# Kernel tuning notes

Measured on AMD Instinct MI355X. Metric: run time of the kernel, lower is better.

The kernel has to match this reference:

```python
import jax, jax.numpy as jnp
import numpy as np

B, N, T, CIN = 16, 400, 12, 2
HID, H, D = 256, 8, 32
P, EMB, TOPK, K = 3, 10, 16, 3


def _conv1d(x, w, b, dil):
    # x: (BN, C, T), w: (O, I, K); causal (left) padding like F.pad((pad,0))
    pad = (K - 1) * dil
    y = jax.lax.conv_general_dilated(x, w, (1,), [(pad, 0)], rhs_dilation=(dil,),
                                     dimension_numbers=('NCH', 'OIH', 'NCH'))
    return y + b[None, :, None]


def _ln(x, g, b):
    m = x.mean(-1, keepdims=True)
    v = x.var(-1, keepdims=True)
    return (x - m) / jnp.sqrt(v + 1e-5) * g + b


def setup_inputs() -> dict:
    key = jax.random.key(0)
    kit = iter(jax.random.split(key, 64))

    def g(shape, s=0.05):
        return jax.random.normal(next(kit), shape, jnp.float32) * s

    # fixed graph: ring with 8 neighbors + self loop -> L = 9*N edges
    idx = np.arange(N)
    offs = np.array([-4, -3, -2, -1, 0, 1, 2, 3, 4])
    recv = np.repeat(idx, offs.size)
    send = (recv + np.tile(offs, N)) % N
    L = recv.size

    inp = {
        'x': g((B, N, T, CIN), 1.0),
        'edge_feat': g((B, L, 2), 1.0),
        'fixed_edge_index': jnp.asarray(np.stack([recv, send]).astype(np.int32)),
        # GTCN layer 0 (dilation 1): gate/filter/skip convs + LayerNorm
        'wg0': g((HID, CIN, K)), 'bg0': jnp.zeros((HID,), jnp.float32),
        'wf0': g((HID, CIN, K)), 'bf0': jnp.zeros((HID,), jnp.float32),
        'ws0': g((HID, CIN, K)), 'bs0': jnp.zeros((HID,), jnp.float32),
        'ln0g': jnp.ones((HID,), jnp.float32), 'ln0b': jnp.zeros((HID,), jnp.float32),
        # GTCN layer 1 (dilation 2)
        'wg1': g((HID, HID, K)), 'bg1': jnp.zeros((HID,), jnp.float32),
        'wf1': g((HID, HID, K)), 'bf1': jnp.zeros((HID,), jnp.float32),
        'ws1': g((HID, HID, K)), 'bs1': jnp.zeros((HID,), jnp.float32),
        'ln1g': jnp.ones((HID,), jnp.float32), 'ln1b': jnp.zeros((HID,), jnp.float32),
        'wsk': g((CIN, HID)), 'bsk': jnp.zeros((HID,), jnp.float32),
        # sparse GAT on fixed physical graph (with 2-dim edge features)
        'sWq': g((HID, HID)), 'sWk': g((HID, HID)), 'sWv': g((HID, HID)),
        'sWe': g((2, HID)),
        'saq': g((H, D)), 'sak': g((H, D)), 'sae': g((H, D)),
        # dense GAT on adaptive adjacency
        'dWq': g((HID, HID)), 'dWk': g((HID, HID)), 'dWv': g((HID, HID)),
        'daq': g((H, D)), 'dak': g((H, D)),
        'E1': g((N, EMB), 0.5), 'E2': g((N, EMB), 0.5),
        # gated fusion
        'fW1': g((HID, HID)), 'fb1': jnp.zeros((HID,), jnp.float32),
        'fW2': g((HID, HID)), 'fb2': jnp.zeros((HID,), jnp.float32),
        'fW3': g((HID, HID)), 'fb3': jnp.zeros((HID,), jnp.float32),
        # prediction head
        'Wo': g((HID, P)), 'bo': jnp.zeros((P,), jnp.float32),
    }
    return inp


def reference(x, edge_feat,
              wg0, bg0, wf0, bf0, ws0, bs0, ln0g, ln0b,
              wg1, bg1, wf1, bf1, ws1, bs1, ln1g, ln1b, wsk, bsk,
              sWq, sWk, sWv, sWe, saq, sak, sae,
              dWq, dWk, dWv, daq, dak, E1, E2,
              fW1, fb1, fW2, fb2, fW3, fb3, Wo, bo,
              fixed_edge_index):
    Bb, Nn, Tt, _ = x.shape
    # ---- GTCN (gated temporal conv stack with residual skip) ----
    res = x @ wsk + bsk                                   # (B,N,T,HID)
    xc = x.reshape(Bb * Nn, Tt, -1).transpose(0, 2, 1)    # (BN,C,T)
    for (wg, bg, wf, bf, ws, bs, lg, lb), dil in (
            ((wg0, bg0, wf0, bf0, ws0, bs0, ln0g, ln0b), 1),
            ((wg1, bg1, wf1, bf1, ws1, bs1, ln1g, ln1b), 2)):
        gate = jax.nn.sigmoid(_conv1d(xc, wg, bg, dil))
        y = gate * _conv1d(xc, wf, bf, dil) + (1 - gate) * _conv1d(xc, ws, bs, dil)
        y = jax.nn.relu(_ln(y.transpose(0, 2, 1), lg, lb))  # (BN,T,HID)
        xc = y.transpose(0, 2, 1)
    h = xc.transpose(0, 2, 1).reshape(Bb, Nn, Tt, HID) + res
    hl = h[:, :, -1, :]                                   # (B,N,HID) last step

    # ---- sparse GAT on fixed physical graph (edge features) ----
    recv, send = fixed_edge_index[0], fixed_edge_index[1]
    q = (hl @ sWq).reshape(Bb, Nn, H, D)
    k = (hl @ sWk).reshape(Bb, Nn, H, D)
    v = (hl @ sWv).reshape(Bb, Nn, H, D)
    e = (edge_feat @ sWe).reshape(Bb, -1, H, D)
    s = (q[:, recv] * saq).sum(-1) + (k[:, send] * sak).sum(-1) + (e * sae).sum(-1)
    s = jax.nn.leaky_relu(s, 0.2)                         # (B,L,H)
    mx = jnp.full((Bb, Nn, H), -jnp.inf, s.dtype).at[:, recv].max(s)
    ex = jnp.exp(s - mx[:, recv])
    den = jnp.zeros((Bb, Nn, H), s.dtype).at[:, recv].add(ex)
    alpha = ex / jnp.clip(den[:, recv], 1e-12, None)
    agg = jnp.zeros((Bb, Nn, H, D), v.dtype).at[:, recv].add(alpha[..., None] * v[:, send])
    h_fixed = jax.nn.elu(agg.reshape(Bb, Nn, HID))

    # ---- dense GAT on adaptive (learned, top-k sparsified) adjacency ----
    A = jax.nn.softmax(jax.nn.relu(E1 @ E2.T), axis=-1)   # (N,N)
    kth = jax.lax.top_k(A, TOPK)[0][:, -1:]
    adj_adp = jnp.where(A >= kth, A, 0.0)
    q = (hl @ dWq).reshape(Bb, Nn, H, D)
    k = (hl @ dWk).reshape(Bb, Nn, H, D)
    v = (hl @ dWv).reshape(Bb, Nn, H, D)
    sc = (q * daq).sum(-1)[:, :, None, :] + (k * dak).sum(-1)[:, None, :, :]  # (B,N,N,H)
    sc = jax.nn.leaky_relu(sc, 0.2)
    sc = sc + jnp.log(jnp.clip(adj_adp, 1e-12, None))[None, :, :, None]      # log-adj trick
    sc = jnp.where((adj_adp > 0)[None, :, :, None], sc, -1e9)
    al = jax.nn.softmax(sc, axis=2)
    h_adp = jax.nn.elu(jnp.einsum('bnjh,bjhd->bnhd', al, v).reshape(Bb, Nn, HID))

    # ---- gated fusion + prediction head ----
    gate = jax.nn.sigmoid((h_fixed + h_adp) @ fW1 + fb1)
    fused = jnp.tanh(gate * (h_fixed @ fW2 + fb2) + (1 - gate) * (h_adp @ fW3 + fb3))
    return fused @ Wo + bo                                # (B,N,P)
```

## Files before the change

### kernel.cpp

```cpp
#include <hip/hip_runtime.h>
#include <math.h>

#define LL 3600
#define NODES 6400

typedef __attribute__((ext_vector_type(8))) _Float16 half8;
typedef __attribute__((ext_vector_type(4))) float f32x4;
typedef __attribute__((ext_vector_type(4))) unsigned short ushort4v;

__device__ __forceinline__ unsigned short f2h(float f) {
    union { _Float16 h; unsigned short u; } cv;
    cv.h = (_Float16)f;
    return cv.u;
}
__device__ __forceinline__ float h2f(unsigned short u) {
    union { unsigned short u; _Float16 h; } cv;
    cv.u = u;
    return (float)cv.h;
}

#define GLOAD16(gp, lp) __builtin_amdgcn_global_load_lds( \
    (const __attribute__((address_space(1))) unsigned int*)(const void*)(gp), \
    (__attribute__((address_space(3))) unsigned int*)(void*)(lp), 16, 0, 0)

__global__ __launch_bounds__(256) void prep_kernel(
    const float* __restrict__ wg1, const float* __restrict__ wf1, const float* __restrict__ ws1,
    const float* __restrict__ sWv, const float* __restrict__ dWv,
    const float* __restrict__ sWq, const float* __restrict__ saq,
    const float* __restrict__ sWk, const float* __restrict__ sak,
    const float* __restrict__ dWq, const float* __restrict__ daq,
    const float* __restrict__ dWk, const float* __restrict__ dak,
    const float* __restrict__ fW1, const float* __restrict__ fW2, const float* __restrict__ fW3,
    const float* __restrict__ sWe, const float* __restrict__ sae,
    const float* __restrict__ E1, const float* __restrict__ E2,
    const float* __restrict__ x,
    const float* __restrict__ wg0, const float* __restrict__ bg0,
    const float* __restrict__ wf0, const float* __restrict__ bf0,
    const float* __restrict__ ws0, const float* __restrict__ bs0,
    const float* __restrict__ lg0, const float* __restrict__ lb0,
    const float* __restrict__ bo,
    unsigned short* __restrict__ W1h,
    unsigned short* __restrict__ W2h,
    unsigned short* __restrict__ W3h,
    float* __restrict__ AeS,
    int* __restrict__ cnt, int* __restrict__ idxs, float* __restrict__ logv,
    unsigned short* __restrict__ Xh,
    float* __restrict__ out) {
    int bid = blockIdx.x;
    int tid = threadIdx.x;

    if (bid < 2304) {
        int idx = bid * 256 + tid;
        int n = idx / 768, k = idx % 768;
        int which = n >> 8, o = n & 255;
        int tt = k >> 8, i = k & 255;
        const float* w = which == 0 ? wg1 : (which == 1 ? wf1 : ws1);
        W1h[idx] = f2h(w[(o * 256 + i) * 3 + tt]);
    } else if (bid < 2944) {
        int idx = (bid - 2304) * 256 + tid;
        int n = idx / 256, k = idx % 256;
        float v = 0.f;
        if (n < 256) v = sWv[k * 256 + n];
        else if (n < 512) v = dWv[k * 256 + (n - 256)];
        else if (n < 544) {
            int j = n - 512, g = j >> 3, h = j & 7;
            const float* Wm = g == 0 ? sWq : (g == 1 ? sWk : (g == 2 ? dWq : dWk));
            const float* am = g == 0 ? saq : (g == 1 ? sak : (g == 2 ? daq : dak));
            float s = 0.f;
            for (int d = 0; d < 32; d++) s += Wm[k * 256 + h * 32 + d] * am[h * 32 + d];
            v = s;
        }
        W2h[idx] = f2h(v);
    } else if (bid < 4480) {
        int idx = (bid - 2944) * 256 + tid;
        int n = idx / 512, k = idx % 512;
        float v = 0.f;
        if (k < 256) {
            if (n < 256) v = fW1[k * 256 + n];
            else if (n < 512) v = fW2[k * 256 + (n - 256)];
        } else {
            int c = k - 256;
            if (n < 256) v = fW1[c * 256 + n];
            else if (n >= 512) v = fW3[c * 256 + (n - 512)];
        }
        W3h[idx] = f2h(v);
    } else if (bid == 4480) {
        if (tid < 16) {
            int cc = tid / 8, h = tid % 8;
            float s = 0.f;
            for (int d = 0; d < 32; d++) s += sWe[cc * 256 + h * 32 + d] * sae[h * 32 + d];
            AeS[tid] = s;
        }
    } else if (bid < 4581) {
        int n = ((bid - 4481) * 256 + tid) >> 6;
        int lane = tid & 63;
        if (n >= 400) return;
        float e1[10];
        #pragma unroll
        for (int k = 0; k < 10; k++) e1[k] = E1[n * 10 + k];
        float p[7];
        #pragma unroll
        for (int i = 0; i < 7; i++) {
            int j = i * 64 + lane;
            if (j < 400) {
                float s = 0.f;
                #pragma unroll
                for (int k = 0; k < 10; k++) s += e1[k] * E2[j * 10 + k];
                p[i] = fmaxf(s, 0.f);
            } else p[i] = -1e30f;
        }
        float mx = -1e30f;
        #pragma unroll
        for (int i = 0; i < 7; i++) mx = fmaxf(mx, p[i]);
        #pragma unroll
        for (int o = 32; o > 0; o >>= 1) mx = fmaxf(mx, __shfl_xor(mx, o, 64));
        float sum = 0.f;
        #pragma unroll
        for (int i = 0; i < 7; i++) {
            int j = i * 64 + lane;
            if (j < 400) { p[i] = expf(p[i] - mx); sum += p[i]; }
        }
        #pragma unroll
        for (int o = 32; o > 0; o >>= 1) sum += __shfl_xor(sum, o, 64);
        float inv = 1.f / sum;
        float m[7];
        #pragma unroll
        for (int i = 0; i < 7; i++) {
            int j = i * 64 + lane;
            if (j < 400) { p[i] *= inv; m[i] = p[i]; }
            else m[i] = -1e30f;
        }
        for (int it = 0; it < 15; ++it) {
            float lm = m[0];
            #pragma unroll
            for (int i = 1; i < 7; i++) lm = fmaxf(lm, m[i]);
            float gm = lm;
            #pragma unroll
            for (int o = 32; o > 0; o >>= 1) gm = fmaxf(gm, __shfl_xor(gm, o, 64));
            unsigned long long msk = __ballot(lm == gm);
            int first = (int)(__ffsll((long long)msk)) - 1;
            if (lane == first) {
                #pragma unroll
                for (int i = 0; i < 7; i++) {
                    if (m[i] == gm) { m[i] = -1e30f; break; }
                }
            }
        }
        float kth = m[0];
        #pragma unroll
        for (int i = 1; i < 7; i++) kth = fmaxf(kth, m[i]);
        #pragma unroll
        for (int o = 32; o > 0; o >>= 1) kth = fmaxf(kth, __shfl_xor(kth, o, 64));
        int base = 0;
        #pragma unroll
        for (int i = 0; i < 7; i++) {
            int j = i * 64 + lane;
            bool pred = (j < 400) && (p[i] >= kth);
            unsigned long long msk = __ballot(pred);
            int pre = __popcll(msk & ((lane == 63) ? 0x7fffffffffffffffull : ((1ull << lane) - 1)));
            if (pred) {
                int pos = base + pre;
                if (pos < 64) {
                    idxs[n * 64 + pos] = j;
                    logv[n * 64 + pos] = logf(fmaxf(p[i], 1e-12f));
                }
            }
            base += __popcll(msk);
        }
        if (lane == 0) cnt[n] = base < 64 ? base : 64;
    } else if (bid < 6181) {
        int lane = tid & 63;
        int node = (bid - 4581) * 4 + (tid >> 6);
        float xs[14];
        #pragma unroll
        for (int t = 0; t < 7; t++) {
            xs[t * 2]     = x[(size_t)(node * 12 + 5 + t) * 2];
            xs[t * 2 + 1] = x[(size_t)(node * 12 + 5 + t) * 2 + 1];
        }
        float wg[4][6], wf[4][6], wsv[4][6], bgv[4], bfv[4], bsv[4], gln[4], bln[4];
        #pragma unroll
        for (int cc = 0; cc < 4; cc++) {
            int o = lane * 4 + cc;
            #pragma unroll
            for (int i = 0; i < 6; i++) {
                wg[cc][i] = wg0[o * 6 + i];
                wf[cc][i] = wf0[o * 6 + i];
                wsv[cc][i] = ws0[o * 6 + i];
            }
            bgv[cc] = bg0[o]; bfv[cc] = bf0[o]; bsv[cc] = bs0[o];
            gln[cc] = lg0[o]; bln[cc] = lb0[o];
        }
        #pragma unroll
        for (int tt = 0; tt < 3; tt++) {
            int tb = 2 * tt;
            float y[4];
            float s1 = 0.f, s2 = 0.f;
            #pragma unroll
            for (int cc = 0; cc < 4; cc++) {
                float g = bgv[cc], f = bfv[cc], s = bsv[cc];
                #pragma unroll
                for (int k = 0; k < 3; k++) {
                    #pragma unroll
                    for (int c = 0; c < 2; c++) {
                        float xv = xs[(tb + k) * 2 + c];
                        g += wg[cc][c * 3 + k] * xv;
                        f += wf[cc][c * 3 + k] * xv;
                        s += wsv[cc][c * 3 + k] * xv;
                    }
                }
                float gate = 1.f / (1.f + expf(-g));
                y[cc] = gate * f + (1.f - gate) * s;
                s1 += y[cc];
                s2 += y[cc] * y[cc];
            }
            #pragma unroll
            for (int o = 32; o > 0; o >>= 1) {
                s1 += __shfl_xor(s1, o, 64);
                s2 += __shfl_xor(s2, o, 64);
            }
            float mean = s1 * (1.f / 256.f);
            float var = s2 * (1.f / 256.f) - mean * mean;
            float rstd = rsqrtf(var + 1e-5f);
            unsigned short h4[4];
            #pragma unroll
            for (int cc = 0; cc < 4; cc++) {
                float v = (y[cc] - mean) * rstd * gln[cc] + bln[cc];
                h4[cc] = f2h(fmaxf(v, 0.f));
            }
            unsigned long long pack = (unsigned long long)h4[0] | ((unsigned long long)h4[1] << 16)
                                    | ((unsigned long long)h4[2] << 32) | ((unsigned long long)h4[3] << 48);
            *(unsigned long long*)&Xh[(size_t)node * 768 + tt * 256 + lane * 4] = pack;
        }
    } else {
        int idx = (bid - 6181) * 256 + tid;
        if (idx < NODES * 3) out[idx] = bo[idx % 3];
    }
}

template<int K, int LDC, int GX, int GY>
__global__ __launch_bounds__(256, 4) void gemm_f16_big(
    const unsigned short* __restrict__ A,
    const unsigned short* __restrict__ BT,
    unsigned short* __restrict__ C) {
    __shared__ __align__(16) unsigned short lA[3][128 * 32];
    __shared__ __align__(16) unsigned short lB[3][64 * 32];
    int tid = threadIdx.x;
    int lane = tid & 63;
    int w = tid >> 6;
    int wm = w >> 1, wn = w & 1;
    int r = lane & 15, g4 = lane >> 4;

    constexpr int NWG = GX * GY;
    constexpr int Q = NWG / 8, R = NWG % 8;
    int flat = blockIdx.y * GX + blockIdx.x;
    int xcd = flat & 7, idx = flat >> 3;
    int nf = (xcd < R ? xcd * (Q + 1) : R * (Q + 1) + (xcd - R) * Q) + idx;
    int col0 = (nf % GX) * 64;
    int row0 = (nf / GX) * 128;

    f32x4 acc[4][2] = {};

    int rS = tid >> 2;
    int slot = tid & 3;
    int tkA0 = (slot ^ (rS & 3)) * 8;
    int tkA1 = (slot ^ ((rS + 64) & 3)) * 8;
    int tkB = tkA0;

#define STAGE(sel, kk) do { \
    GLOAD16(A + (size_t)(row0 + rS) * K + (kk) + tkA0, &lA[sel][tid * 8]); \
    GLOAD16(A + (size_t)(row0 + 64 + rS) * K + (kk) + tkA1, &lA[sel][(tid + 256) * 8]); \
    GLOAD16(BT + (size_t)(col0 + rS) * K + (kk) + tkB, &lB[sel][tid * 8]); \
} while (0)

    int sw = (g4 ^ (r & 3)) << 3;

#define COMPUTE(cur) do { \
    half8 a_[4], b_[2]; \
    _Pragma("unroll") \
    for (int mi = 0; mi < 4; ++mi) \
        a_[mi] = *(const half8*)&lA[cur][(wm * 64 + mi * 16 + r) * 32 + sw]; \
    _Pragma("unroll") \
    for (int ni = 0; ni < 2; ++ni) \
        b_[ni] = *(const half8*)&lB[cur][(wn * 32 + ni * 16 + r) * 32 + sw]; \
    _Pragma("unroll") \
    for (int mi = 0; mi < 4; ++mi) \
        _Pragma("unroll") \
        for (int ni = 0; ni < 2; ++ni) \
            acc[mi][ni] = __builtin_amdgcn_mfma_f32_16x16x32_f16(a_[mi], b_[ni], acc[mi][ni], 0, 0, 0); \
} while (0)

    constexpr int NT = K >> 5;
    STAGE(0, 0);
    STAGE(1, 32);
    for (int t = 0; t < NT - 1; ++t) {
        asm volatile("s_waitcnt vmcnt(3)" ::: "memory");
        __builtin_amdgcn_s_barrier();
        if (t + 2 < NT) STAGE((t + 2) % 3, (t + 2) * 32);
        COMPUTE(t % 3);
    }
    asm volatile("s_waitcnt vmcnt(0)" ::: "memory");
    __builtin_amdgcn_s_barrier();
    COMPUTE((NT - 1) % 3);
#undef STAGE
#undef COMPUTE

    #pragma unroll
    for (int mi = 0; mi < 4; ++mi) {
        #pragma unroll
        for (int ni = 0; ni < 2; ++ni) {
            int rowb = row0 + wm * 64 + mi * 16 + g4 * 4;
            int colb = col0 + wn * 32 + ni * 16 + r;
            #pragma unroll
            for (int j = 0; j < 4; ++j)
                C[(size_t)(rowb + j) * LDC + colb] = f2h(acc[mi][ni][j]);
        }
    }
}

__global__ __launch_bounds__(256, 3) void gemm3_fused(
    const unsigned short* __restrict__ A,
    const unsigned short* __restrict__ BT,
    const float* __restrict__ fb1, const float* __restrict__ fb2, const float* __restrict__ fb3,
    const float* __restrict__ Wo,
    float* __restrict__ out) {
    __shared__ __align__(16) unsigned short lA[3][64 * 32];
    __shared__ __align__(16) unsigned short lB[3][3][64 * 32];
    int tid = threadIdx.x;
    int lane = tid & 63;
    int w = tid >> 6;
    int wm = w >> 1, wn = w & 1;
    int r = lane & 15, g4 = lane >> 4;

    constexpr int NWG = 400;
    constexpr int Q = NWG / 8;
    int flat = blockIdx.y * 4 + blockIdx.x;
    int xcd = flat & 7, idx = flat >> 3;
    int nf = xcd * Q + idx;
    int c0 = (nf % 4) * 64;
    int row0 = (nf / 4) * 64;

    f32x4 acc[3][2][2] = {};

    int rS = tid >> 2;
    int slot = tid & 3;
    int tk = (slot ^ (rS & 3)) * 8;

#define STAGE3(sel, kk) do { \
    GLOAD16(A + (size_t)(row0 + rS) * 512 + (kk) + tk, &lA[sel][tid * 8]); \
    GLOAD16(BT + (size_t)(c0 + rS) * 512 + (kk) + tk, &lB[sel][0][tid * 8]); \
    GLOAD16(BT + (size_t)(c0 + 256 + rS) * 512 + (kk) + tk, &lB[sel][1][tid * 8]); \
    GLOAD16(BT + (size_t)(c0 + 512 + rS) * 512 + (kk) + tk, &lB[sel][2][tid * 8]); \
} while (0)

    int sw = (g4 ^ (r & 3)) << 3;

#define COMPUTE3(cur) do { \
    half8 a_[2], b_[3][2]; \
    _Pragma("unroll") \
    for (int mi = 0; mi < 2; ++mi) \
        a_[mi] = *(const half8*)&lA[cur][(wm * 32 + mi * 16 + r) * 32 + sw]; \
    _Pragma("unroll") \
    for (int q = 0; q < 3; ++q) \
        _Pragma("unroll") \
        for (int ni = 0; ni < 2; ++ni) \
            b_[q][ni] = *(const half8*)&lB[cur][q][(wn * 32 + ni * 16 + r) * 32 + sw]; \
    _Pragma("unroll") \
    for (int q = 0; q < 3; ++q) \
        _Pragma("unroll") \
        for (int mi = 0; mi < 2; ++mi) \
            _Pragma("unroll") \
            for (int ni = 0; ni < 2; ++ni) \
                acc[q][mi][ni] = __builtin_amdgcn_mfma_f32_16x16x32_f16(a_[mi], b_[q][ni], acc[q][mi][ni], 0, 0, 0); \
} while (0)

    constexpr int NT = 16;
    STAGE3(0, 0);
    STAGE3(1, 32);
    for (int t = 0; t < NT - 1; ++t) {
        asm volatile("s_waitcnt vmcnt(4)" ::: "memory");
        __builtin_amdgcn_s_barrier();
        if (t + 2 < NT) STAGE3((t + 2) % 3, (t + 2) * 32);
        COMPUTE3(t % 3);
    }
    asm volatile("s_waitcnt vmcnt(0)" ::: "memory");
    __builtin_amdgcn_s_barrier();
    COMPUTE3((NT - 1) % 3);
#undef STAGE3
#undef COMPUTE3

    #pragma unroll
    for (int mi = 0; mi < 2; ++mi) {
        float v0[4] = {}, v1[4] = {}, v2[4] = {};
        #pragma unroll
        for (int ni = 0; ni < 2; ++ni) {
            int ch = c0 + wn * 32 + ni * 16 + r;
            float b1 = fb1[ch], b2 = fb2[ch], b3 = fb3[ch];
            float w0 = Wo[ch * 3 + 0], w1 = Wo[ch * 3 + 1], w2 = Wo[ch * 3 + 2];
            #pragma unroll
            for (int j = 0; j < 4; ++j) {
                float g = 1.f / (1.f + expf(-(acc[0][mi][ni][j] + b1)));
                float a2 = acc[1][mi][ni][j] + b2;
                float a3 = acc[2][mi][ni][j] + b3;
                float fused = tanhf(g * a2 + (1.f - g) * a3);
                v0[j] += fused * w0;
                v1[j] += fused * w1;
                v2[j] += fused * w2;
            }
        }
        #pragma unroll
        for (int off = 1; off < 16; off <<= 1) {
            #pragma unroll
            for (int j = 0; j < 4; ++j) {
                v0[j] += __shfl_xor(v0[j], off, 64);
                v1[j] += __shfl_xor(v1[j], off, 64);
                v2[j] += __shfl_xor(v2[j], off, 64);
            }
        }
        if (r == 0) {
            int rowb = row0 + wm * 32 + mi * 16 + g4 * 4;
            #pragma unroll
            for (int j = 0; j < 4; ++j) {
                atomicAdd(&out[(size_t)(rowb + j) * 3 + 0], v0[j]);
                atomicAdd(&out[(size_t)(rowb + j) * 3 + 1], v1[j]);
                atomicAdd(&out[(size_t)(rowb + j) * 3 + 2], v2[j]);
            }
        }
    }
}

__global__ __launch_bounds__(256) void epi1_kernel(
    const unsigned short* __restrict__ Y1, const float* __restrict__ x,
    const float* __restrict__ bg1, const float* __restrict__ bf1, const float* __restrict__ bs1,
    const float* __restrict__ lg, const float* __restrict__ lb,
    const float* __restrict__ wsk, const float* __restrict__ bsk,
    unsigned short* __restrict__ HLh) {
    int lane = threadIdx.x & 63;
    int node = blockIdx.x * 4 + (threadIdx.x >> 6);
    size_t base = (size_t)node * 768;
    ushort4v yg = *(const ushort4v*)&Y1[base + lane * 4];
    ushort4v yf = *(const ushort4v*)&Y1[base + 256 + lane * 4];
    ushort4v ys = *(const ushort4v*)&Y1[base + 512 + lane * 4];
    float y[4];
    float s1 = 0.f, s2 = 0.f;
    #pragma unroll
    for (int cc = 0; cc < 4; cc++) {
        int o = lane * 4 + cc;
        float g = h2f(yg[cc]) + bg1[o];
        float f = h2f(yf[cc]) + bf1[o];
        float s = h2f(ys[cc]) + bs1[o];
        float gate = 1.f / (1.f + expf(-g));
        y[cc] = gate * f + (1.f - gate) * s;
        s1 += y[cc];
        s2 += y[cc] * y[cc];
    }
    #pragma unroll
    for (int off = 32; off > 0; off >>= 1) {
        s1 += __shfl_xor(s1, off, 64);
        s2 += __shfl_xor(s2, off, 64);
    }
    float mean = s1 * (1.f / 256.f);
    float var = s2 * (1.f / 256.f) - mean * mean;
    float rstd = rsqrtf(var + 1e-5f);
    float x0 = x[(size_t)(node * 12 + 11) * 2];
    float x1 = x[(size_t)(node * 12 + 11) * 2 + 1];
    unsigned short h4[4];
    #pragma unroll
    for (int cc = 0; cc < 4; cc++) {
        int o = lane * 4 + cc;
        float v = (y[cc] - mean) * rstd * lg[o] + lb[o];
        v = fmaxf(v, 0.f);
        float res = x0 * wsk[o] + x1 * wsk[256 + o] + bsk[o];
        h4[cc] = f2h(v + res);
    }
    unsigned long long pack = (unsigned long long)h4[0] | ((unsigned long long)h4[1] << 16)
                            | ((unsigned long long)h4[2] << 32) | ((unsigned long long)h4[3] << 48);
    *(unsigned long long*)&HLh[(size_t)node * 256 + lane * 4] = pack;
}

__global__ __launch_bounds__(256) void gat_kernel(
    const unsigned short* __restrict__ Y2, const float* __restrict__ ef,
    const int* __restrict__ fei, const float* __restrict__ AeS,
    const int* __restrict__ cnt, const int* __restrict__ idxs, const float* __restrict__ logv,
    unsigned short* __restrict__ Uh) {
    int node = (blockIdx.x & 7) * 800 + (blockIdx.x >> 3);
    int b = node / 400, n = node % 400;
    int tid = threadIdx.x;
    __shared__ int snd[9];
    __shared__ float alf[9][8];
    __shared__ float invdf[8];
    __shared__ int jidx[64];
    __shared__ float sca[64][8];
    __shared__ float alb[64][8];
    __shared__ float invda[8];
    __shared__ float svf[9][8];
    int c = cnt[n];

    if (tid < 64) {
        int lane = tid;
        if (lane < 9) snd[lane] = fei[LL + n * 9 + lane];
        for (int e = lane; e < 72; e += 64) {
            int j = e >> 3, h = e & 7;
            int l = n * 9 + j;
            float e0 = ef[((size_t)b * LL + l) * 2];
            float e1 = ef[((size_t)b * LL + l) * 2 + 1];
            float ae = e0 * AeS[h] + e1 * AeS[8 + h];
            float aq = h2f(Y2[(size_t)node * 640 + 512 + h]);
            float ak = h2f(Y2[((size_t)(b * 400 + snd[j])) * 640 + 520 + h]);
            float s = aq + ak + ae;
            svf[j][h] = s > 0.f ? s : 0.2f * s;
        }
        if (lane < 8) {
            int h = lane;
            float mx = -1e30f;
            #pragma unroll
            for (int j = 0; j < 9; j++) mx = fmaxf(mx, svf[j][h]);
            float den = 0.f;
            #pragma unroll
            for (int j = 0; j < 9; j++) { float e = expf(svf[j][h] - mx); alf[j][h] = e; den += e; }
            invdf[h] = 1.f / fmaxf(den, 1e-12f);
        }
    } else if (tid < 128) {
        int lane = tid - 64;
        if (lane < c) jidx[lane] = idxs[n * 64 + lane];
        float jl = (lane < c) ? logv[n * 64 + lane] : 0.f;
        for (int e = lane; e < c * 8; e += 64) {
            int j = e >> 3, h = e & 7;
            float aq = h2f(Y2[(size_t)node * 640 + 528 + h]);
            float ak = h2f(Y2[((size_t)(b * 400 + jidx[j])) * 640 + 536 + h]);
            float s = aq + ak;
            s = s > 0.f ? s : 0.2f * s;
            sca[j][h] = s + __shfl(jl, j, 64);
        }
        int h = lane >> 3, grp = lane & 7;
        float mx = -1e30f;
        for (int j = grp; j < c; j += 8) mx = fmaxf(mx, sca[j][h]);
        #pragma unroll
        for (int o = 1; o < 8; o <<= 1) mx = fmaxf(mx, __shfl_xor(mx, o, 64));
        float s = 0.f;
        for (int j = grp; j < c; j += 8) { float e = expf(sca[j][h] - mx); alb[j][h] = e; s += e; }
        #pragma unroll
        for (int o = 1; o < 8; o <<= 1) s += __shfl_xor(s, o, 64);
        if (grp == 0) invda[h] = 1.f / s;
    }
    __syncthreads();

    if (tid < 128) {
        int ch = tid * 2;
        int h = ch >> 5;
        float a0 = 0.f, a1 = 0.f;
        #pragma unroll
        for (int j = 0; j < 9; j++) {
            unsigned v = *(const unsigned*)&Y2[((size_t)(b * 400 + snd[j])) * 640 + ch];
            float al = alf[j][h];
            a0 += al * h2f((unsigned short)(v & 0xffff));
            a1 += al * h2f((unsigned short)(v >> 16));
        }
        float iv = invdf[h];
        a0 *= iv; a1 *= iv;
        a0 = a0 > 0.f ? a0 : (expf(a0) - 1.f);
        a1 = a1 > 0.f ? a1 : (expf(a1) - 1.f);
        unsigned o = (unsigned)f2h(a0) | ((unsigned)f2h(a1) << 16);
        *(unsigned*)&Uh[(size_t)node * 512 + ch] = o;
    } else {
        int ch = (tid - 128) * 2;
        int h = ch >> 5;
        float a0 = 0.f, a1 = 0.f;
        for (int j = 0; j < c; j++) {
            unsigned v = *(const unsigned*)&Y2[((size_t)(b * 400 + jidx[j])) * 640 + 256 + ch];
            float al = alb[j][h];
            a0 += al * h2f((unsigned short)(v & 0xffff));
            a1 += al * h2f((unsigned short)(v >> 16));
        }
        float iv = invda[h];
        a0 *= iv; a1 *= iv;
        a0 = a0 > 0.f ? a0 : (expf(a0) - 1.f);
        a1 = a1 > 0.f ? a1 : (expf(a1) - 1.f);
        unsigned o = (unsigned)f2h(a0) | ((unsigned)f2h(a1) << 16);
        *(unsigned*)&Uh[(size_t)node * 512 + 256 + ch] = o;
    }
}

extern "C" void kernel_launch(void* const* d_in, const int* in_sizes, int n_in,
                              void* d_out, int out_size, void* d_ws, size_t ws_size,
                              hipStream_t stream) {
    const float* x   = (const float*)d_in[0];
    const float* ef  = (const float*)d_in[1];
    const int*   fei = (const int*)d_in[2];
    const float* wg0 = (const float*)d_in[3];
    const float* bg0 = (const float*)d_in[4];
    const float* wf0 = (const float*)d_in[5];
    const float* bf0 = (const float*)d_in[6];
    const float* ws0 = (const float*)d_in[7];
    const float* bs0 = (const float*)d_in[8];
    const float* ln0g = (const float*)d_in[9];
    const float* ln0b = (const float*)d_in[10];
    const float* wg1 = (const float*)d_in[11];
    const float* bg1 = (const float*)d_in[12];
    const float* wf1 = (const float*)d_in[13];
    const float* bf1 = (const float*)d_in[14];
    const float* ws1 = (const float*)d_in[15];
    const float* bs1 = (const float*)d_in[16];
    const float* ln1g = (const float*)d_in[17];
    const float* ln1b = (const float*)d_in[18];
    const float* wsk = (const float*)d_in[19];
    const float* bsk = (const float*)d_in[20];
    const float* sWq = (const float*)d_in[21];
    const float* sWk = (const float*)d_in[22];
    const float* sWv = (const float*)d_in[23];
    const float* sWe = (const float*)d_in[24];
    const float* saq = (const float*)d_in[25];
    const float* sak = (const float*)d_in[26];
    const float* sae = (const float*)d_in[27];
    const float* dWq = (const float*)d_in[28];
    const float* dWk = (const float*)d_in[29];
    const float* dWv = (const float*)d_in[30];
    const float* daq = (const float*)d_in[31];
    const float* dak = (const float*)d_in[32];
    const float* E1  = (const float*)d_in[33];
    const float* E2  = (const float*)d_in[34];
    const float* fW1 = (const float*)d_in[35];
    const float* fb1 = (const float*)d_in[36];
    const float* fW2 = (const float*)d_in[37];
    const float* fb2 = (const float*)d_in[38];
    const float* fW3 = (const float*)d_in[39];
    const float* fb3 = (const float*)d_in[40];
    const float* Wo  = (const float*)d_in[41];
    const float* bo  = (const float*)d_in[42];
    float* out = (float*)d_out;

    char* b = (char*)d_ws;
    unsigned short* Xh  = (unsigned short*)(b + 0);
    unsigned short* Yh  = (unsigned short*)(b + 9830400);
    unsigned short* HLh = (unsigned short*)(b + 19660800);
    unsigned short* Uh  = (unsigned short*)(b + 22937600);
    unsigned short* W1h = (unsigned short*)(b + 29491200);
    unsigned short* W2h = (unsigned short*)(b + 30670848);
    unsigned short* W3h = (unsigned short*)(b + 30998528);
    float*          AES = (float*)(b + 31784960);
    float*          LOGV= (float*)(b + 31785216);
    int*            CNT = (int*)(b + 31887616);
    int*            IDX = (int*)(b + 31889216);

    prep_kernel<<<6256, 256, 0, stream>>>(
        wg1, wf1, ws1,
        sWv, dWv, sWq, saq, sWk, sak, dWq, daq, dWk, dak,
        fW1, fW2, fW3, sWe, sae, E1, E2,
        x, wg0, bg0, wf0, bf0, ws0, bs0, ln0g, ln0b, bo,
        W1h, W2h, W3h, AES,
        CNT, IDX, LOGV, Xh, out);

    gemm_f16_big<768, 768, 12, 50><<<dim3(12, 50), 256, 0, stream>>>(Xh, W1h, Yh);

    epi1_kernel<<<1600, 256, 0, stream>>>(Yh, x, bg1, bf1, bs1, ln1g, ln1b, wsk, bsk, HLh);

    gemm_f16_big<256, 640, 9, 50><<<dim3(9, 50), 256, 0, stream>>>(HLh, W2h, Yh);

    gat_kernel<<<NODES, 256, 0, stream>>>(Yh, ef, fei, AES, CNT, IDX, LOGV, Uh);

    gemm3_fused<<<dim3(4, 100), 256, 0, stream>>>(Uh, W3h, fb1, fb2, fb3, Wo, out);
}
```

Before: 94.01 us.

## Retile GEMMs to 64x64 with K=64 stages and unroll dense-GAT gather

The two big fp16 GEMMs move from 128x64 tiles with 32-wide K stages to 64x64 tiles with 64-wide K stages and an 8-slot XOR swizzle, doubling the grid. The aim is more workgroups on the 256 CUs and fewer barriers per K. The cost is less reuse of each tile and a larger LDS footprint, with launch bounds lowered to 3 blocks. The dense-GAT aggregation loop is also unrolled by four with separate accumulators to expose more independent gather loads.

```diff
diff --git a/kernel.cpp b/kernel.cpp
--- a/kernel.cpp
+++ b/kernel.cpp
@@ -238,12 +238,12 @@
 }
 
 template<int K, int LDC, int GX, int GY>
-__global__ __launch_bounds__(256, 4) void gemm_f16_big(
+__global__ __launch_bounds__(256, 3) void gemm_f16_k64(
     const unsigned short* __restrict__ A,
     const unsigned short* __restrict__ BT,
     unsigned short* __restrict__ C) {
-    __shared__ __align__(16) unsigned short lA[3][128 * 32];
-    __shared__ __align__(16) unsigned short lB[3][64 * 32];
+    __shared__ __align__(16) unsigned short lA[3][64 * 64];
+    __shared__ __align__(16) unsigned short lB[3][64 * 64];
     int tid = threadIdx.x;
     int lane = tid & 63;
     int w = tid >> 6;
@@ -256,46 +256,48 @@
     int xcd = flat & 7, idx = flat >> 3;
     int nf = (xcd < R ? xcd * (Q + 1) : R * (Q + 1) + (xcd - R) * Q) + idx;
     int col0 = (nf % GX) * 64;
-    int row0 = (nf / GX) * 128;
-
-    f32x4 acc[4][2] = {};
-
-    int rS = tid >> 2;
-    int slot = tid & 3;
-    int tkA0 = (slot ^ (rS & 3)) * 8;
-    int tkA1 = (slot ^ ((rS + 64) & 3)) * 8;
-    int tkB = tkA0;
+    int row0 = (nf / GX) * 64;
+
+    f32x4 acc[2][2] = {};
+
+    int rA0 = tid >> 3, sl0 = tid & 7;
+    int rA1 = 32 + (tid >> 3);
+    int tk0 = (sl0 ^ (rA0 & 7)) * 8;
+    int tk1 = (sl0 ^ (rA1 & 7)) * 8;
 
 #define STAGE(sel, kk) do { \
-    GLOAD16(A + (size_t)(row0 + rS) * K + (kk) + tkA0, &lA[sel][tid * 8]); \
-    GLOAD16(A + (size_t)(row0 + 64 + rS) * K + (kk) + tkA1, &lA[sel][(tid + 256) * 8]); \
-    GLOAD16(BT + (size_t)(col0 + rS) * K + (kk) + tkB, &lB[sel][tid * 8]); \
+    GLOAD16(A + (size_t)(row0 + rA0) * K + (kk) + tk0, &lA[sel][(rA0 * 8 + sl0) * 8]); \
+    GLOAD16(A + (size_t)(row0 + rA1) * K + (kk) + tk1, &lA[sel][(rA1 * 8 + sl0) * 8]); \
+    GLOAD16(BT + (size_t)(col0 + rA0) * K + (kk) + tk0, &lB[sel][(rA0 * 8 + sl0) * 8]); \
+    GLOAD16(BT + (size_t)(col0 + rA1) * K + (kk) + tk1, &lB[sel][(rA1 * 8 + sl0) * 8]); \
 } while (0)
 
-    int sw = (g4 ^ (r & 3)) << 3;
-
 #define COMPUTE(cur) do { \
-    half8 a_[4], b_[2]; \
     _Pragma("unroll") \
-    for (int mi = 0; mi < 4; ++mi) \
-        a_[mi] = *(const half8*)&lA[cur][(wm * 64 + mi * 16 + r) * 32 + sw]; \
-    _Pragma("unroll") \
-    for (int ni = 0; ni < 2; ++ni) \
-        b_[ni] = *(const half8*)&lB[cur][(wn * 32 + ni * 16 + r) * 32 + sw]; \
-    _Pragma("unroll") \
-    for (int mi = 0; mi < 4; ++mi) \
+    for (int ks = 0; ks < 2; ++ks) { \
+        int sw = ((ks * 4 + g4) ^ (r & 7)) << 3; \
+        half8 a_[2], b_[2]; \
+        _Pragma("unroll") \
+        for (int mi = 0; mi < 2; ++mi) \
+            a_[mi] = *(const half8*)&lA[cur][(wm * 32 + mi * 16 + r) * 64 + sw]; \
         _Pragma("unroll") \
         for (int ni = 0; ni < 2; ++ni) \
-            acc[mi][ni] = __builtin_amdgcn_mfma_f32_16x16x32_f16(a_[mi], b_[ni], acc[mi][ni], 0, 0, 0); \
+            b_[ni] = *(const half8*)&lB[cur][(wn * 32 + ni * 16 + r) * 64 + sw]; \
+        _Pragma("unroll") \
+        for (int mi = 0; mi < 2; ++mi) \
+            _Pragma("unroll") \
+            for (int ni = 0; ni < 2; ++ni) \
+                acc[mi][ni] = __builtin_amdgcn_mfma_f32_16x16x32_f16(a_[mi], b_[ni], acc[mi][ni], 0, 0, 0); \
+    } \
 } while (0)
 
-    constexpr int NT = K >> 5;
+    constexpr int NT = K >> 6;
     STAGE(0, 0);
-    STAGE(1, 32);
+    STAGE(1, 64);
     for (int t = 0; t < NT - 1; ++t) {
-        asm volatile("s_waitcnt vmcnt(3)" ::: "memory");
+        asm volatile("s_waitcnt vmcnt(4)" ::: "memory");
         __builtin_amdgcn_s_barrier();
-        if (t + 2 < NT) STAGE((t + 2) % 3, (t + 2) * 32);
+        if (t + 2 < NT) STAGE((t + 2) % 3, (t + 2) * 64);
         COMPUTE(t % 3);
     }
     asm volatile("s_waitcnt vmcnt(0)" ::: "memory");
@@ -305,10 +307,10 @@
 #undef COMPUTE
 
     #pragma unroll
-    for (int mi = 0; mi < 4; ++mi) {
+    for (int mi = 0; mi < 2; ++mi) {
         #pragma unroll
         for (int ni = 0; ni < 2; ++ni) {
-            int rowb = row0 + wm * 64 + mi * 16 + g4 * 4;
+            int rowb = row0 + wm * 32 + mi * 16 + g4 * 4;
             int colb = col0 + wn * 32 + ni * 16 + r;
             #pragma unroll
             for (int j = 0; j < 4; ++j)
@@ -564,13 +566,32 @@
     } else {
         int ch = (tid - 128) * 2;
         int h = ch >> 5;
-        float a0 = 0.f, a1 = 0.f;
-        for (int j = 0; j < c; j++) {
+        float p0a = 0.f, p0b = 0.f, p1a = 0.f, p1b = 0.f;
+        float p2a = 0.f, p2b = 0.f, p3a = 0.f, p3b = 0.f;
+        int j = 0;
+        for (; j + 4 <= c; j += 4) {
+            unsigned v0 = *(const unsigned*)&Y2[((size_t)(b * 400 + jidx[j])) * 640 + 256 + ch];
+            unsigned v1 = *(const unsigned*)&Y2[((size_t)(b * 400 + jidx[j + 1])) * 640 + 256 + ch];
+            unsigned v2 = *(const unsigned*)&Y2[((size_t)(b * 400 + jidx[j + 2])) * 640 + 256 + ch];
+            unsigned v3 = *(const unsigned*)&Y2[((size_t)(b * 400 + jidx[j + 3])) * 640 + 256 + ch];
+            float l0 = alb[j][h], l1 = alb[j + 1][h], l2 = alb[j + 2][h], l3 = alb[j + 3][h];
+            p0a += l0 * h2f((unsigned short)(v0 & 0xffff));
+            p0b += l0 * h2f((unsigned short)(v0 >> 16));
+            p1a += l1 * h2f((unsigned short)(v1 & 0xffff));
+            p1b += l1 * h2f((unsigned short)(v1 >> 16));
+            p2a += l2 * h2f((unsigned short)(v2 & 0xffff));
+            p2b += l2 * h2f((unsigned short)(v2 >> 16));
+            p3a += l3 * h2f((unsigned short)(v3 & 0xffff));
+            p3b += l3 * h2f((unsigned short)(v3 >> 16));
+        }
+        for (; j < c; j++) {
             unsigned v = *(const unsigned*)&Y2[((size_t)(b * 400 + jidx[j])) * 640 + 256 + ch];
             float al = alb[j][h];
-            a0 += al * h2f((unsigned short)(v & 0xffff));
-            a1 += al * h2f((unsigned short)(v >> 16));
-        }
+            p0a += al * h2f((unsigned short)(v & 0xffff));
+            p0b += al * h2f((unsigned short)(v >> 16));
+        }
+        float a0 = (p0a + p1a) + (p2a + p3a);
+        float a1 = (p0b + p1b) + (p2b + p3b);
         float iv = invda[h];
         a0 *= iv; a1 *= iv;
         a0 = a0 > 0.f ? a0 : (expf(a0) - 1.f);
@@ -649,11 +670,11 @@
         W1h, W2h, W3h, AES,
         CNT, IDX, LOGV, Xh, out);
 
-    gemm_f16_big<768, 768, 12, 50><<<dim3(12, 50), 256, 0, stream>>>(Xh, W1h, Yh);
+    gemm_f16_k64<768, 768, 12, 100><<<dim3(12, 100), 256, 0, stream>>>(Xh, W1h, Yh);
 
     epi1_kernel<<<1600, 256, 0, stream>>>(Yh, x, bg1, bf1, bs1, ln1g, ln1b, wsk, bsk, HLh);
 
-    gemm_f16_big<256, 640, 9, 50><<<dim3(9, 50), 256, 0, stream>>>(HLh, W2h, Yh);
+    gemm_f16_k64<256, 640, 9, 100><<<dim3(9, 100), 256, 0, stream>>>(HLh, W2h, Yh);
 
     gat_kernel<<<NODES, 256, 0, stream>>>(Yh, ef, fei, AES, CNT, IDX, LOGV, Uh);
 
```

After: 92.97 us, median of 2. No clear change (-1.1%).
